# Optimization experiments

Hardware: AMD Instinct MI355X
Metric: run time of the kernel (lower is better)

## Reference

```python
import jax, jax.numpy as jnp
import numpy as np

E = 256      # embedding_dim
H = 8        # num_heads
D = E // H   # head_dim = 32
F = 1024     # dim_feedforward
EPS = 1e-5


def layer_norm(x, gamma, beta):
    mu = jnp.mean(x, axis=-1, keepdims=True)
    var = jnp.var(x, axis=-1, keepdims=True)
    return (x - mu) * jax.lax.rsqrt(var + EPS) * gamma + beta


def setup_inputs() -> dict:
    key = jax.random.key(0)
    ks = jax.random.split(key, 12)
    s = lambda fan_in: 1.0 / np.sqrt(fan_in)
    src = jax.random.normal(ks[0], (4, 2048, E), dtype=jnp.float32)
    w_in = jax.random.uniform(ks[1], (3 * E, E), minval=-s(E), maxval=s(E), dtype=jnp.float32)
    w_out = jax.random.uniform(ks[2], (E, E), minval=-s(E), maxval=s(E), dtype=jnp.float32)
    w1 = jax.random.uniform(ks[3], (F, E), minval=-s(E), maxval=s(E), dtype=jnp.float32)
    b1 = jax.random.uniform(ks[4], (F,), minval=-s(E), maxval=s(E), dtype=jnp.float32)
    w2 = jax.random.uniform(ks[5], (E, F), minval=-s(F), maxval=s(F), dtype=jnp.float32)
    b2 = jax.random.uniform(ks[6], (E,), minval=-s(F), maxval=s(F), dtype=jnp.float32)
    g1 = jnp.ones((E,), jnp.float32)
    beta1 = jnp.zeros((E,), jnp.float32)
    g2 = jnp.ones((E,), jnp.float32)
    beta2 = jnp.zeros((E,), jnp.float32)
    return {"src": src, "w_in": w_in, "w_out": w_out, "w1": w1, "b1": b1,
            "w2": w2, "b2": b2, "g1": g1, "beta1": beta1, "g2": g2, "beta2": beta2}


def reference(src, w_in, w_out, w1, b1, w2, b2, g1, beta1, g2, beta2):
    B, S, _ = src.shape
    scale = D ** (-0.5)
    # --- pre-norm self-attention block ---
    x = layer_norm(src, g1, beta1)                 # [B,S,E]
    qkv = x @ w_in.T                               # [B,S,3E]
    q, k, v = jnp.split(qkv, 3, axis=-1)
    q = q.reshape(B, S, H, D).transpose(0, 2, 1, 3)  # [B,H,S,D]
    k = k.reshape(B, S, H, D).transpose(0, 2, 1, 3)
    v = v.reshape(B, S, H, D).transpose(0, 2, 1, 3)
    scores = jnp.einsum('bhqd,bhkd->bhqk', q, k) * scale  # [B,H,S,S]
    attn = jax.nn.softmax(scores, axis=-1)
    out = jnp.einsum('bhqk,bhkd->bhqd', attn, v)   # [B,H,S,D]
    out = out.transpose(0, 2, 1, 3).reshape(B, S, E)
    src = src + out @ w_out.T
    # --- pre-norm FFN block ---
    y = layer_norm(src, g2, beta2)
    y = jax.nn.relu(y @ w1.T + b1) @ w2.T + b2
    return src + y
```

## Files before the change

kernel.cpp:

```cpp
#include <hip/hip_runtime.h>
#include <hip/hip_bf16.h>
#include <math.h>

typedef unsigned short u16;
typedef unsigned int   u32;
using bf16x8 = __attribute__((ext_vector_type(8))) short;
using f32x4  = __attribute__((ext_vector_type(4))) float;

#define TE 256
#define TH 8
#define TS 2048
#define TB 4
#define NTOK 8192
#define QSCALE 0.2550120651552454f
#define EXP2(x) __builtin_amdgcn_exp2f(x)

__device__ __forceinline__ void async16(const u16* g, u16* l) {
    __builtin_amdgcn_global_load_lds(
        (const __attribute__((address_space(1))) u32*)g,
        (__attribute__((address_space(3))) u32*)l, 16, 0, 0);
}
__device__ __forceinline__ u32 pkbf(float a, float b) {
    u32 ua = __float_as_uint(a) + 0x8000u;
    u32 ub = __float_as_uint(b) + 0x8000u;
    return __builtin_amdgcn_perm(ub, ua, 0x07060302u);
}

__global__ __launch_bounds__(256) void ln_bf(const float* __restrict__ in,
        u16* __restrict__ out, const float* __restrict__ gamma,
        const float* __restrict__ beta) {
    int row  = blockIdx.x * 4 + (threadIdx.x >> 6);
    int lane = threadIdx.x & 63;
    float4 v = ((const float4*)(in + (size_t)row * TE))[lane];
    float s  = v.x + v.y + v.z + v.w;
    float s2 = v.x*v.x + v.y*v.y + v.z*v.z + v.w*v.w;
    #pragma unroll
    for (int off = 32; off > 0; off >>= 1) {
        s  += __shfl_down(s,  off, 64);
        s2 += __shfl_down(s2, off, 64);
    }
    s  = __shfl(s,  0, 64);
    s2 = __shfl(s2, 0, 64);
    float mu = s * (1.f / TE);
    float rs = rsqrtf(s2 * (1.f / TE) - mu * mu + 1e-5f);
    float4 g = ((const float4*)gamma)[lane];
    float4 b = ((const float4*)beta )[lane];
    u32 lo = pkbf((v.x - mu) * rs * g.x + b.x, (v.y - mu) * rs * g.y + b.y);
    u32 hi = pkbf((v.z - mu) * rs * g.z + b.z, (v.w - mu) * rs * g.w + b.w);
    ((uint2*)(out + (size_t)row * TE))[lane] = make_uint2(lo, hi);
}

__global__ __launch_bounds__(256) void convw(const float* __restrict__ s0, u16* d0,
        const float* __restrict__ s1, u16* d1, const float* __restrict__ s2, u16* d2,
        const float* __restrict__ s3, u16* d3) {
    int i = (blockIdx.x * 256 + threadIdx.x) * 4;
    const float* s; u16* d;
    if      (i < 196608) { s = s0; d = d0; }
    else if (i < 262144) { s = s1; d = d1; i -= 196608; }
    else if (i < 524288) { s = s2; d = d2; i -= 262144; }
    else                 { s = s3; d = d3; i -= 524288; }
    float4 v = *(const float4*)(s + i);
    *(uint2*)(d + i) = make_uint2(pkbf(v.x, v.y), pkbf(v.z, v.w));
}

template<int K, int BM, int EPI>
__global__ __launch_bounds__(256) void mgemm(const u16* __restrict__ A,
        const u16* __restrict__ W, const float* __restrict__ bias,
        const float* __restrict__ R, float* __restrict__ Cf,
        u16* __restrict__ Cb, int M) {
    constexpr int BN = BM;
    __shared__ u16 Al[2][BM * 32];
    __shared__ u16 Wl[2][BN * 32];
    const int tid = threadIdx.x, w = tid >> 6, l = tid & 63;
    const int n0 = blockIdx.y * BM;
    const int m0 = blockIdx.x * BN;
    constexpr int NT = (BM == 128) ? 4 : 2;
    constexpr int NF = (BM == 128) ? 4 : 2;
    const int tw = (w & 1) * NT * 16;
    const int fw = (w >> 1) * NF * 16;
    const int fr = l & 15, fq = l >> 4;
    const int sr = l >> 2, sc = (l & 3) * 8;
    f32x4 acc[NT][NF];
    #pragma unroll
    for (int t = 0; t < NT; t++)
        #pragma unroll
        for (int f = 0; f < NF; f++)
            #pragma unroll
            for (int r = 0; r < 4; r++) acc[t][f][r] = 0.f;

    for (int k0 = 0; k0 < K; k0 += 64) {
        __syncthreads();
        #pragma unroll
        for (int hh = 0; hh < 2; hh++) {
            const int kc = k0 + hh * 32;
            if (BM == 128) {
                #pragma unroll
                for (int c = 0; c < 2; c++) {
                    int rr = (w * 2 + c) * 16 + sr;
                    async16(A + (size_t)(n0 + rr) * K + kc + sc, &Al[hh][(w * 2 + c) * 512]);
                    async16(W + (size_t)(m0 + rr) * K + kc + sc, &Wl[hh][(w * 2 + c) * 512]);
                }
            } else {
                int rr = w * 16 + sr;
                async16(A + (size_t)(n0 + rr) * K + kc + sc, &Al[hh][w * 512]);
                async16(W + (size_t)(m0 + rr) * K + kc + sc, &Wl[hh][w * 512]);
            }
        }
        __syncthreads();
        #pragma unroll
        for (int hh = 0; hh < 2; hh++) {
            bf16x8 af[NT], wf[NF];
            #pragma unroll
            for (int t = 0; t < NT; t++)
                af[t] = *(const bf16x8*)&Al[hh][(tw + t * 16 + fr) * 32 + fq * 8];
            #pragma unroll
            for (int f = 0; f < NF; f++)
                wf[f] = *(const bf16x8*)&Wl[hh][(fw + f * 16 + fr) * 32 + fq * 8];
            #pragma unroll
            for (int t = 0; t < NT; t++)
                #pragma unroll
                for (int f = 0; f < NF; f++)
                    acc[t][f] = __builtin_amdgcn_mfma_f32_16x16x32_bf16(
                        wf[f], af[t], acc[t][f], 0, 0, 0);
        }
    }
    #pragma unroll
    for (int t = 0; t < NT; t++) {
        const int tok = n0 + tw + t * 16 + fr;
        #pragma unroll
        for (int f = 0; f < NF; f++) {
            const int fb = m0 + fw + f * 16 + fq * 4;
            f32x4 v = acc[t][f];
            if (EPI == 0) {
                const float qs = (fb < 256) ? QSCALE : 1.f;
                *(uint2*)(Cb + (size_t)tok * M + fb) =
                    make_uint2(pkbf(v[0]*qs, v[1]*qs), pkbf(v[2]*qs, v[3]*qs));
            } else if (EPI == 1) {
                float4 r4 = *(const float4*)(R + (size_t)tok * M + fb);
                *(float4*)(Cf + (size_t)tok * M + fb) =
                    make_float4(v[0]+r4.x, v[1]+r4.y, v[2]+r4.z, v[3]+r4.w);
            } else if (EPI == 2) {
                float4 b4 = *(const float4*)(bias + fb);
                *(uint2*)(Cb + (size_t)tok * M + fb) = make_uint2(
                    pkbf(fmaxf(v[0]+b4.x, 0.f), fmaxf(v[1]+b4.y, 0.f)),
                    pkbf(fmaxf(v[2]+b4.z, 0.f), fmaxf(v[3]+b4.w, 0.f)));
            } else {
                float4 b4 = *(const float4*)(bias + fb);
                float4 r4 = *(const float4*)(R + (size_t)tok * M + fb);
                *(float4*)(Cf + (size_t)tok * M + fb) = make_float4(
                    v[0]+b4.x+r4.x, v[1]+b4.y+r4.y, v[2]+b4.z+r4.z, v[3]+b4.w+r4.w);
            }
        }
    }
}

__global__ __launch_bounds__(256) void attn_k(const u16* __restrict__ qkv,
        u16* __restrict__ attn) {
    const int bh = blockIdx.x, b = bh >> 3, h = bh & 7;
    const int q0 = blockIdx.y * 64;
    const int tid = threadIdx.x, w = tid >> 6, l = tid & 63;
    const int qw = w & 1, kw = w >> 1;
    const int fr = l & 15, fq = l >> 4;
    const size_t btok = (size_t)b * TS;

    __shared__ u16 Vt[2][4 * 1296];
    __shared__ u16 Pl[4][32 * 40];

    bf16x8 qf[2];
    #pragma unroll
    for (int qs = 0; qs < 2; qs++)
        qf[qs] = *(const bf16x8*)(qkv +
            (btok + q0 + qw * 32 + qs * 16 + fr) * 768 + h * 32 + fq * 8);

    f32x4 o[2][2];
    #pragma unroll
    for (int ds = 0; ds < 2; ds++)
        #pragma unroll
        for (int qs = 0; qs < 2; qs++)
            #pragma unroll
            for (int r = 0; r < 4; r++) o[ds][qs][r] = 0.f;
    float ps[2] = {0.f, 0.f};

    u16* Pw = Pl[w];
    const int vkv = l * 2, vd0 = qw * 16;
    const u16* kbase = qkv + btok * 768 + 256 + h * 32;
    const int kvbase = kw * 1024;

    for (int it = 0; it < 8; it++) {
        const int kv0 = kvbase + it * 128;
        __syncthreads();
        {
            const u16* va = qkv + (btok + kv0 + vkv) * 768 + 512 + h * 32 + vd0;
            uint4 ra0 = *(const uint4*)va;
            uint4 ra1 = *(const uint4*)(va + 8);
            uint4 rb0 = *(const uint4*)(va + 768);
            uint4 rb1 = *(const uint4*)(va + 776);
            const u16* pa0 = (const u16*)&ra0; const u16* pa1 = (const u16*)&ra1;
            const u16* pb0 = (const u16*)&rb0; const u16* pb1 = (const u16*)&rb1;
            u16* vb_ = &Vt[kw][(vkv >> 5) * 1296 + (vkv & 31)];
            #pragma unroll
            for (int i = 0; i < 8; i++) {
                *(u32*)&vb_[(vd0 + i) * 40]     = (u32)pa0[i] | ((u32)pb0[i] << 16);
                *(u32*)&vb_[(vd0 + 8 + i) * 40] = (u32)pa1[i] | ((u32)pb1[i] << 16);
            }
        }
        __syncthreads();
        #pragma unroll
        for (int sub = 0; sub < 4; sub++) {
            const u16* krow = kbase + (size_t)(kv0 + sub * 32) * 768;
            bf16x8 kf0 = *(const bf16x8*)(krow + (size_t)fr * 768 + fq * 8);
            bf16x8 kf1 = *(const bf16x8*)(krow + (size_t)(16 + fr) * 768 + fq * 8);
            f32x4 z; z[0] = z[1] = z[2] = z[3] = 0.f;
            #pragma unroll
            for (int qs = 0; qs < 2; qs++) {
                f32x4 st0 = __builtin_amdgcn_mfma_f32_16x16x32_bf16(kf0, qf[qs], z, 0, 0, 0);
                f32x4 st1 = __builtin_amdgcn_mfma_f32_16x16x32_bf16(kf1, qf[qs], z, 0, 0, 0);
                float p0[4], p1[4];
                #pragma unroll
                for (int r = 0; r < 4; r++) { p0[r] = EXP2(st0[r]); p1[r] = EXP2(st1[r]); }
                ps[qs] += ((p0[0]+p0[1]) + (p0[2]+p0[3]))
                        + ((p1[0]+p1[1]) + (p1[2]+p1[3]));
                u16* prow = &Pw[(qs * 16 + fr) * 40];
                *(uint2*)&prow[fq * 4]      = make_uint2(pkbf(p0[0],p0[1]), pkbf(p0[2],p0[3]));
                *(uint2*)&prow[16 + fq * 4] = make_uint2(pkbf(p1[0],p1[1]), pkbf(p1[2],p1[3]));
            }
            bf16x8 pf0 = *(const bf16x8*)&Pw[fr * 40 + fq * 8];
            bf16x8 pf1 = *(const bf16x8*)&Pw[(16 + fr) * 40 + fq * 8];
            bf16x8 vf0 = *(const bf16x8*)&Vt[kw][sub * 1296 + fr * 40 + fq * 8];
            bf16x8 vf1 = *(const bf16x8*)&Vt[kw][sub * 1296 + (16 + fr) * 40 + fq * 8];
            o[0][0] = __builtin_amdgcn_mfma_f32_16x16x32_bf16(vf0, pf0, o[0][0], 0, 0, 0);
            o[0][1] = __builtin_amdgcn_mfma_f32_16x16x32_bf16(vf0, pf1, o[0][1], 0, 0, 0);
            o[1][0] = __builtin_amdgcn_mfma_f32_16x16x32_bf16(vf1, pf0, o[1][0], 0, 0, 0);
            o[1][1] = __builtin_amdgcn_mfma_f32_16x16x32_bf16(vf1, pf1, o[1][1], 0, 0, 0);
        }
    }
    #pragma unroll
    for (int qs = 0; qs < 2; qs++) {
        ps[qs] += __shfl_xor(ps[qs], 16, 64);
        ps[qs] += __shfl_xor(ps[qs], 32, 64);
    }
    __syncthreads();
    float* mrg = (float*)&Vt[0][0];
    if (kw == 1) {
        float* p = mrg + (qw * 64 + l) * 18;
        #pragma unroll
        for (int ds = 0; ds < 2; ds++)
            #pragma unroll
            for (int qs = 0; qs < 2; qs++)
                #pragma unroll
                for (int r = 0; r < 4; r++) p[ds * 8 + qs * 4 + r] = o[ds][qs][r];
        p[16] = ps[0]; p[17] = ps[1];
    }
    __syncthreads();
    if (kw == 0) {
        const float* p = mrg + (qw * 64 + l) * 18;
        #pragma unroll
        for (int ds = 0; ds < 2; ds++)
            #pragma unroll
            for (int qs = 0; qs < 2; qs++)
                #pragma unroll
                for (int r = 0; r < 4; r++) o[ds][qs][r] += p[ds * 8 + qs * 4 + r];
        ps[0] += p[16]; ps[1] += p[17];
        #pragma unroll
        for (int qs = 0; qs < 2; qs++) {
            float inv = 1.f / ps[qs];
            int tok = (int)btok + q0 + qw * 32 + qs * 16 + fr;
            #pragma unroll
            for (int ds = 0; ds < 2; ds++) {
                *(uint2*)(attn + (size_t)tok * 256 + h * 32 + ds * 16 + fq * 4) =
                    make_uint2(pkbf(o[ds][qs][0]*inv, o[ds][qs][1]*inv),
                               pkbf(o[ds][qs][2]*inv, o[ds][qs][3]*inv));
            }
        }
    }
}

extern "C" void kernel_launch(void* const* d_in, const int* in_sizes, int n_in,
                              void* d_out, int out_size, void* d_ws, size_t ws_size,
                              hipStream_t stream) {
    const float* src  = (const float*)d_in[0];
    const float* w_in = (const float*)d_in[1];
    const float* w_out= (const float*)d_in[2];
    const float* w1   = (const float*)d_in[3];
    const float* b1   = (const float*)d_in[4];
    const float* w2   = (const float*)d_in[5];
    const float* b2   = (const float*)d_in[6];
    const float* g1   = (const float*)d_in[7];
    const float* be1  = (const float*)d_in[8];
    const float* g2   = (const float*)d_in[9];
    const float* be2  = (const float*)d_in[10];
    float* out = (float*)d_out;

    u16* xb    = (u16*)d_ws;
    u16* qkvb  = xb + (size_t)NTOK * 256;
    u16* attnb = xb;
    u16* h1b   = (u16*)d_ws;
    u16* x2b   = (u16*)((char*)d_ws + (size_t)NTOK * 1024 * 2);
    u16* wib   = x2b + (size_t)NTOK * 256;
    u16* wob   = wib + 768 * 256;
    u16* w1b   = wob + 256 * 256;
    u16* w2b   = w1b + 1024 * 256;

    convw<<<768, 256, 0, stream>>>(w_in, wib, w_out, wob, w1, w1b, w2, w2b);
    ln_bf<<<NTOK / 4, 256, 0, stream>>>(src, xb, g1, be1);
    mgemm<256, 128, 0><<<dim3(6, 64), 256, 0, stream>>>(
        xb, wib, nullptr, nullptr, nullptr, qkvb, 768);
    attn_k<<<dim3(32, 32), 256, 0, stream>>>(qkvb, attnb);
    mgemm<256, 64, 1><<<dim3(4, 128), 256, 0, stream>>>(
        attnb, wob, nullptr, src, out, nullptr, 256);
    ln_bf<<<NTOK / 4, 256, 0, stream>>>(out, x2b, g2, be2);
    mgemm<256, 128, 2><<<dim3(8, 64), 256, 0, stream>>>(
        x2b, w1b, b1, nullptr, nullptr, h1b, 1024);
    mgemm<1024, 64, 3><<<dim3(4, 128), 256, 0, stream>>>(
        h1b, w2b, b2, out, out, nullptr, 256);
}
```

Before: 195.9 us.

## Replace tiled GEMM with weight-stationary LDS GEMM, split-K atomics, and prefetch K in attention

The double-buffered A/W tiled GEMM is replaced by a weight-stationary kernel. Each block loads a full weight slice into padded LDS once, then streams activation rows straight from global memory into MFMA fragments. The final FFN GEMM is split across K into two halves that accumulate into the output with float atomics. Separately, attention now prefetches K two chunks ahead and computes the next chunk's scores before the current P·V step, to hide global-load latency. The risks are uncoalesced direct global A loads, atomic contention, and nondeterministic summation order.

```diff
diff --git a/kernel.cpp b/kernel.cpp
--- a/kernel.cpp
+++ b/kernel.cpp
@@ -15,11 +15,6 @@
 #define QSCALE 0.2550120651552454f
 #define EXP2(x) __builtin_amdgcn_exp2f(x)
 
-__device__ __forceinline__ void async16(const u16* g, u16* l) {
-    __builtin_amdgcn_global_load_lds(
-        (const __attribute__((address_space(1))) u32*)g,
-        (__attribute__((address_space(3))) u32*)l, 16, 0, 0);
-}
 __device__ __forceinline__ u32 pkbf(float a, float b) {
     u32 ua = __float_as_uint(a) + 0x8000u;
     u32 ub = __float_as_uint(b) + 0x8000u;
@@ -63,73 +58,66 @@
     *(uint2*)(d + i) = make_uint2(pkbf(v.x, v.y), pkbf(v.z, v.w));
 }
 
-template<int K, int BM, int EPI>
-__global__ __launch_bounds__(256) void mgemm(const u16* __restrict__ A,
+template<int K, int Kc, int NFEAT, int NF, int EPI>
+__global__ __launch_bounds__(256) void wgemm(const u16* __restrict__ A,
         const u16* __restrict__ W, const float* __restrict__ bias,
         const float* __restrict__ R, float* __restrict__ Cf,
         u16* __restrict__ Cb, int M) {
-    constexpr int BN = BM;
-    __shared__ u16 Al[2][BM * 32];
-    __shared__ u16 Wl[2][BN * 32];
+    constexpr int LROW = Kc + 8;
+    __shared__ u16 Wl[NFEAT * LROW];
     const int tid = threadIdx.x, w = tid >> 6, l = tid & 63;
-    const int n0 = blockIdx.y * BM;
-    const int m0 = blockIdx.x * BN;
-    constexpr int NT = (BM == 128) ? 4 : 2;
-    constexpr int NF = (BM == 128) ? 4 : 2;
-    const int tw = (w & 1) * NT * 16;
-    const int fw = (w >> 1) * NF * 16;
     const int fr = l & 15, fq = l >> 4;
-    const int sr = l >> 2, sc = (l & 3) * 8;
-    f32x4 acc[NT][NF];
-    #pragma unroll
-    for (int t = 0; t < NT; t++)
+    int slice, koff;
+    if (EPI == 3) { slice = blockIdx.x >> 1; koff = (blockIdx.x & 1) * Kc; }
+    else          { slice = blockIdx.x;      koff = 0; }
+    const int fbase = slice * NFEAT;
+    const int tok0 = blockIdx.y * 256 + w * 64;
+
+    {
+        constexpr int CH = NFEAT * Kc / 8;
+        #pragma unroll
+        for (int c0 = 0; c0 < CH; c0 += 256) {
+            int c = c0 + tid;
+            int row = c / (Kc / 8), cp = c % (Kc / 8);
+            *(uint4*)&Wl[row * LROW + cp * 8] =
+                *(const uint4*)(W + (size_t)(fbase + row) * K + koff + cp * 8);
+        }
+    }
+    __syncthreads();
+
+    f32x4 acc[4][NF];
+    #pragma unroll
+    for (int t = 0; t < 4; t++)
         #pragma unroll
         for (int f = 0; f < NF; f++)
             #pragma unroll
             for (int r = 0; r < 4; r++) acc[t][f][r] = 0.f;
 
-    for (int k0 = 0; k0 < K; k0 += 64) {
-        __syncthreads();
-        #pragma unroll
-        for (int hh = 0; hh < 2; hh++) {
-            const int kc = k0 + hh * 32;
-            if (BM == 128) {
-                #pragma unroll
-                for (int c = 0; c < 2; c++) {
-                    int rr = (w * 2 + c) * 16 + sr;
-                    async16(A + (size_t)(n0 + rr) * K + kc + sc, &Al[hh][(w * 2 + c) * 512]);
-                    async16(W + (size_t)(m0 + rr) * K + kc + sc, &Wl[hh][(w * 2 + c) * 512]);
-                }
-            } else {
-                int rr = w * 16 + sr;
-                async16(A + (size_t)(n0 + rr) * K + kc + sc, &Al[hh][w * 512]);
-                async16(W + (size_t)(m0 + rr) * K + kc + sc, &Wl[hh][w * 512]);
-            }
-        }
-        __syncthreads();
-        #pragma unroll
-        for (int hh = 0; hh < 2; hh++) {
-            bf16x8 af[NT], wf[NF];
-            #pragma unroll
-            for (int t = 0; t < NT; t++)
-                af[t] = *(const bf16x8*)&Al[hh][(tw + t * 16 + fr) * 32 + fq * 8];
+    const u16* arow0 = A + (size_t)(tok0 + fr) * K + koff;
+    constexpr int STEPS = Kc / 32;
+    #pragma unroll 4
+    for (int s = 0; s < STEPS; s++) {
+        bf16x8 af[4], wf[NF];
+        #pragma unroll
+        for (int t = 0; t < 4; t++)
+            af[t] = *(const bf16x8*)(arow0 + (size_t)t * 16 * K + s * 32 + fq * 8);
+        #pragma unroll
+        for (int f = 0; f < NF; f++)
+            wf[f] = *(const bf16x8*)&Wl[(f * 16 + fr) * LROW + s * 32 + fq * 8];
+        #pragma unroll
+        for (int t = 0; t < 4; t++)
             #pragma unroll
             for (int f = 0; f < NF; f++)
-                wf[f] = *(const bf16x8*)&Wl[hh][(fw + f * 16 + fr) * 32 + fq * 8];
-            #pragma unroll
-            for (int t = 0; t < NT; t++)
-                #pragma unroll
-                for (int f = 0; f < NF; f++)
-                    acc[t][f] = __builtin_amdgcn_mfma_f32_16x16x32_bf16(
-                        wf[f], af[t], acc[t][f], 0, 0, 0);
-        }
-    }
-    #pragma unroll
-    for (int t = 0; t < NT; t++) {
-        const int tok = n0 + tw + t * 16 + fr;
+                acc[t][f] = __builtin_amdgcn_mfma_f32_16x16x32_bf16(
+                    wf[f], af[t], acc[t][f], 0, 0, 0);
+    }
+
+    #pragma unroll
+    for (int t = 0; t < 4; t++) {
+        const int tok = tok0 + t * 16 + fr;
         #pragma unroll
         for (int f = 0; f < NF; f++) {
-            const int fb = m0 + fw + f * 16 + fq * 4;
+            const int fb = fbase + f * 16 + fq * 4;
             f32x4 v = acc[t][f];
             if (EPI == 0) {
                 const float qs = (fb < 256) ? QSCALE : 1.f;
@@ -145,10 +133,14 @@
                     pkbf(fmaxf(v[0]+b4.x, 0.f), fmaxf(v[1]+b4.y, 0.f)),
                     pkbf(fmaxf(v[2]+b4.z, 0.f), fmaxf(v[3]+b4.w, 0.f)));
             } else {
-                float4 b4 = *(const float4*)(bias + fb);
-                float4 r4 = *(const float4*)(R + (size_t)tok * M + fb);
-                *(float4*)(Cf + (size_t)tok * M + fb) = make_float4(
-                    v[0]+b4.x+r4.x, v[1]+b4.y+r4.y, v[2]+b4.z+r4.z, v[3]+b4.w+r4.w);
+                float bb[4] = {0.f, 0.f, 0.f, 0.f};
+                if (koff == 0) {
+                    float4 b4 = *(const float4*)(bias + fb);
+                    bb[0] = b4.x; bb[1] = b4.y; bb[2] = b4.z; bb[3] = b4.w;
+                }
+                float* cp_ = Cf + (size_t)tok * M + fb;
+                #pragma unroll
+                for (int r = 0; r < 4; r++) atomicAdd(cp_ + r, v[r] + bb[r]);
             }
         }
     }
@@ -185,6 +177,24 @@
     const int vkv = l * 2, vd0 = qw * 16;
     const u16* kbase = qkv + btok * 768 + 256 + h * 32;
     const int kvbase = kw * 1024;
+
+#define KLOAD(ci, a_, b_) { \
+        const u16* krow_ = kbase + (size_t)(kvbase + (ci) * 32) * 768; \
+        a_ = *(const bf16x8*)(krow_ + (size_t)fr * 768 + fq * 8); \
+        b_ = *(const bf16x8*)(krow_ + (size_t)(16 + fr) * 768 + fq * 8); }
+
+    bf16x8 kA[2], kB[2];
+    f32x4 st[2][2][2];
+    KLOAD(0, kA[0], kB[0]);
+    KLOAD(1, kA[1], kB[1]);
+    {
+        f32x4 z; z[0] = z[1] = z[2] = z[3] = 0.f;
+        #pragma unroll
+        for (int qs = 0; qs < 2; qs++) {
+            st[0][0][qs] = __builtin_amdgcn_mfma_f32_16x16x32_bf16(kA[0], qf[qs], z, 0, 0, 0);
+            st[0][1][qs] = __builtin_amdgcn_mfma_f32_16x16x32_bf16(kB[0], qf[qs], z, 0, 0, 0);
+        }
+    }
 
     for (int it = 0; it < 8; it++) {
         const int kv0 = kvbase + it * 128;
@@ -207,22 +217,30 @@
         __syncthreads();
         #pragma unroll
         for (int sub = 0; sub < 4; sub++) {
-            const u16* krow = kbase + (size_t)(kv0 + sub * 32) * 768;
-            bf16x8 kf0 = *(const bf16x8*)(krow + (size_t)fr * 768 + fq * 8);
-            bf16x8 kf1 = *(const bf16x8*)(krow + (size_t)(16 + fr) * 768 + fq * 8);
-            f32x4 z; z[0] = z[1] = z[2] = z[3] = 0.f;
+            const int ci = it * 4 + sub;
+            const int p = ci & 1, np = p ^ 1;
+            KLOAD((ci + 2) & 31, kA[p], kB[p]);
             #pragma unroll
             for (int qs = 0; qs < 2; qs++) {
-                f32x4 st0 = __builtin_amdgcn_mfma_f32_16x16x32_bf16(kf0, qf[qs], z, 0, 0, 0);
-                f32x4 st1 = __builtin_amdgcn_mfma_f32_16x16x32_bf16(kf1, qf[qs], z, 0, 0, 0);
                 float p0[4], p1[4];
                 #pragma unroll
-                for (int r = 0; r < 4; r++) { p0[r] = EXP2(st0[r]); p1[r] = EXP2(st1[r]); }
+                for (int r = 0; r < 4; r++) {
+                    p0[r] = EXP2(st[p][0][qs][r]);
+                    p1[r] = EXP2(st[p][1][qs][r]);
+                }
                 ps[qs] += ((p0[0]+p0[1]) + (p0[2]+p0[3]))
                         + ((p1[0]+p1[1]) + (p1[2]+p1[3]));
                 u16* prow = &Pw[(qs * 16 + fr) * 40];
                 *(uint2*)&prow[fq * 4]      = make_uint2(pkbf(p0[0],p0[1]), pkbf(p0[2],p0[3]));
                 *(uint2*)&prow[16 + fq * 4] = make_uint2(pkbf(p1[0],p1[1]), pkbf(p1[2],p1[3]));
+            }
+            {
+                f32x4 z; z[0] = z[1] = z[2] = z[3] = 0.f;
+                #pragma unroll
+                for (int qs = 0; qs < 2; qs++) {
+                    st[np][0][qs] = __builtin_amdgcn_mfma_f32_16x16x32_bf16(kA[np], qf[qs], z, 0, 0, 0);
+                    st[np][1][qs] = __builtin_amdgcn_mfma_f32_16x16x32_bf16(kB[np], qf[qs], z, 0, 0, 0);
+                }
             }
             bf16x8 pf0 = *(const bf16x8*)&Pw[fr * 40 + fq * 8];
             bf16x8 pf1 = *(const bf16x8*)&Pw[(16 + fr) * 40 + fq * 8];
@@ -273,6 +291,7 @@
             }
         }
     }
+#undef KLOAD
 }
 
 extern "C" void kernel_launch(void* const* d_in, const int* in_sizes, int n_in,
@@ -303,14 +322,14 @@
 
     convw<<<768, 256, 0, stream>>>(w_in, wib, w_out, wob, w1, w1b, w2, w2b);
     ln_bf<<<NTOK / 4, 256, 0, stream>>>(src, xb, g1, be1);
-    mgemm<256, 128, 0><<<dim3(6, 64), 256, 0, stream>>>(
+    wgemm<256, 256, 64, 4, 0><<<dim3(12, 32), 256, 0, stream>>>(
         xb, wib, nullptr, nullptr, nullptr, qkvb, 768);
     attn_k<<<dim3(32, 32), 256, 0, stream>>>(qkvb, attnb);
-    mgemm<256, 64, 1><<<dim3(4, 128), 256, 0, stream>>>(
+    wgemm<256, 256, 32, 2, 1><<<dim3(8, 32), 256, 0, stream>>>(
         attnb, wob, nullptr, src, out, nullptr, 256);
     ln_bf<<<NTOK / 4, 256, 0, stream>>>(out, x2b, g2, be2);
-    mgemm<256, 128, 2><<<dim3(8, 64), 256, 0, stream>>>(
+    wgemm<256, 256, 64, 4, 2><<<dim3(16, 32), 256, 0, stream>>>(
         x2b, w1b, b1, nullptr, nullptr, h1b, 1024);
-    mgemm<1024, 64, 3><<<dim3(4, 128), 256, 0, stream>>>(
-        h1b, w2b, b2, out, out, nullptr, 256);
-}
+    wgemm<1024, 512, 32, 2, 3><<<dim3(16, 32), 256, 0, stream>>>(
+        h1b, w2b, b2, nullptr, out, nullptr, 256);
+}
```

New measurement: 250.7 us. 28.0% more time.
